# Optimization experiments

Hardware: AMD Instinct MI355X
Metric: run time of the kernel (lower is better)

The kernel has to match this reference:

```python
import jax, jax.numpy as jnp
import numpy as np

WS = 8
NH = 16
EPS = 1e-5

# relative position index (static, same as the torch buffer)
def _rel_index(ws):
    coords = np.stack(np.meshgrid(np.arange(ws), np.arange(ws), indexing='ij'))  # 2,ws,ws
    flat = coords.reshape(2, -1)
    rel = flat[:, :, None] - flat[:, None, :]
    rel = rel.transpose(1, 2, 0).copy()
    rel[..., 0] += ws - 1
    rel[..., 1] += ws - 1
    rel[..., 0] *= 2 * ws - 1
    return rel.sum(-1)  # (ws*ws, ws*ws)

REL_IDX = jnp.asarray(_rel_index(WS))

def conv2d(x, w, dilation=1, pad=None, groups=1):
    k = w.shape[-1]
    if pad is None:
        pad = (dilation * (k - 1)) // 2
    return jax.lax.conv_general_dilated(
        x, w, (1, 1), ((pad, pad), (pad, pad)), rhs_dilation=(dilation, dilation),
        dimension_numbers=('NCHW', 'OIHW', 'NCHW'), feature_group_count=groups)

def bn(x, p):
    g, b, m, v = p[0], p[1], p[2], p[3]
    inv = g / jnp.sqrt(v + EPS)
    return x * inv[:, None, None] + (b - m * inv)[:, None, None]

def avgpool(x, kh, kw, ph, pw):
    # torch AvgPool2d with count_include_pad=True: zero-pad then divide by kernel size
    s = jax.lax.reduce_window(x, 0.0, jax.lax.add, (1, 1, kh, kw), (1, 1, 1, 1),
                              ((0, 0), (0, 0), (ph, ph), (pw, pw)))
    return s / (kh * kw)

def _fwd(x, w_pre, bn_pre, w_l1, bn_l1, w_l2, bn_l2, w_l3, bn_l3, w_qkv, rpb, w_dw, w_pw, bn_proj):
    B, C, H, W = x.shape
    # local conv branch (chunk 256 -> 86,86,84 with dilations 1,2,3)
    local = bn(conv2d(x, w_pre), bn_pre)
    l1 = bn(conv2d(local[:, :86], w_l1, dilation=1), bn_l1)
    l2 = bn(conv2d(local[:, 86:172], w_l2, dilation=2), bn_l2)
    l3 = bn(conv2d(local[:, 172:], w_l3, dilation=3), bn_l3)
    local = jnp.concatenate([l1, l2, l3], axis=1)
    # pad to window multiple (reflect); static shapes so Python branch is fine
    ph, pw = (-H) % WS, (-W) % WS
    if ph or pw:
        x = jnp.pad(x, ((0, 0), (0, 0), (0, ph), (0, pw)), mode='reflect')
    Hp, Wp = H + ph, W + pw
    hh, ww = Hp // WS, Wp // WS
    d = C // NH
    qkv = conv2d(x, w_qkv)  # (B, 3C, Hp, Wp)
    qkv = qkv.reshape(B, 3, NH, d, hh, WS, ww, WS)
    qkv = qkv.transpose(1, 0, 4, 6, 2, 5, 7, 3).reshape(3, B * hh * ww, NH, WS * WS, d)
    q, k, v = qkv[0], qkv[1], qkv[2]
    dots = jnp.einsum('whid,whjd->whij', q, k) * (d ** -0.5)
    bias = rpb[REL_IDX.reshape(-1)].reshape(WS * WS, WS * WS, NH).transpose(2, 0, 1)
    attn = jax.nn.softmax(dots + bias[None], axis=-1)
    out = jnp.einsum('whij,whjd->whid', attn, v)
    out = out.reshape(B, hh, ww, NH, WS, WS, d).transpose(0, 3, 6, 1, 4, 2, 5).reshape(B, C, Hp, Wp)
    out = out[:, :, :H, :W]
    ax = avgpool(jnp.pad(out, ((0, 0), (0, 0), (0, 1), (0, 0)), mode='reflect'), WS, 1, WS // 2 - 1, 0)
    ay = avgpool(jnp.pad(out, ((0, 0), (0, 0), (0, 0), (0, 1)), mode='reflect'), 1, WS, 0, WS // 2 - 1)
    out = ax + ay + local
    out = jnp.pad(out, ((0, 0), (0, 0), (0, 1), (0, 1)), mode='reflect')
    out = conv2d(out, w_dw, pad=3, groups=C)       # depthwise 8x8
    out = bn(conv2d(out, w_pw), bn_proj)           # pointwise + BN
    return out[:, :, :H, :W]

def setup_inputs() -> dict:
    key = jax.random.key(0)
    ks = jax.random.split(key, 16)
    def w(k, shape, s=0.05):
        return jax.random.normal(k, shape, dtype=jnp.float32) * s
    def bnp(k, c):
        p = jax.random.uniform(k, (4, c), dtype=jnp.float32)
        return p.at[3].add(0.5)  # keep var positive and away from 0
    return {
        'x': jax.random.normal(ks[0], (8, 256, 128, 128), dtype=jnp.float32),
        'w_pre': w(ks[1], (256, 256, 1, 1)), 'bn_pre': bnp(ks[2], 256),
        'w_l1': w(ks[3], (86, 86, 3, 3)), 'bn_l1': bnp(ks[4], 86),
        'w_l2': w(ks[5], (86, 86, 3, 3)), 'bn_l2': bnp(ks[6], 86),
        'w_l3': w(ks[7], (84, 84, 3, 3)), 'bn_l3': bnp(ks[8], 84),
        'w_qkv': w(ks[9], (768, 256, 1, 1)),
        'rpb': w(ks[10], (225, 16), 0.02),
        'w_dw': w(ks[11], (256, 1, 8, 8)),
        'w_pw': w(ks[12], (256, 256, 1, 1)),
        'bn_proj': bnp(ks[13], 256),
    }

def reference(x, w_pre, bn_pre, w_l1, bn_l1, w_l2, bn_l2, w_l3, bn_l3, w_qkv, rpb, w_dw, w_pw, bn_proj):
    return _fwd(x, w_pre, bn_pre, w_l1, bn_l1, w_l2, bn_l2, w_l3, bn_l3, w_qkv, rpb, w_dw, w_pw, bn_proj)
```

## Files before the change

kernel.cpp:

```cpp
#include <hip/hip_runtime.h>
#include <hip/hip_bf16.h>
#include <cstdint>
#include <cstddef>

namespace {

constexpr int HW = 16384;

typedef short vec8s __attribute__((ext_vector_type(8)));
typedef float f32x4 __attribute__((ext_vector_type(4)));

__device__ __forceinline__ float u2f(uint32_t u){ union { uint32_t u; float f; } v; v.u = u; return v.f; }
__device__ __forceinline__ uint32_t f2u(float f){ union { float f; uint32_t u; } v; v.f = f; return v.u; }
__device__ __forceinline__ uint16_t f2bf(float f){
  uint32_t u = f2u(f);
  u += 0x7fffu + ((u >> 16) & 1u);
  return (uint16_t)(u >> 16);
}
__device__ __forceinline__ void unpack2(uint32_t w, float& lo, float& hi){
  lo = u2f(w << 16);
  hi = u2f(w & 0xffff0000u);
}

__global__ __launch_bounds__(256) void k_w2bf(
    const float* __restrict__ src, uint16_t* __restrict__ dst, int n)
{
  int i = (blockIdx.x * 256 + threadIdx.x) * 8;
  if (i + 8 <= n) {
    float4 a = *(const float4*)(src + i);
    float4 b = *(const float4*)(src + i + 4);
    uint4 pk;
    pk.x = (uint32_t)f2bf(a.x) | ((uint32_t)f2bf(a.y) << 16);
    pk.y = (uint32_t)f2bf(a.z) | ((uint32_t)f2bf(a.w) << 16);
    pk.z = (uint32_t)f2bf(b.x) | ((uint32_t)f2bf(b.y) << 16);
    pk.w = (uint32_t)f2bf(b.z) | ((uint32_t)f2bf(b.w) << 16);
    *(uint4*)(dst + i) = pk;
  }
}

template<int OUT_MODE, int NCO, bool WINM>
__global__ __launch_bounds__(256) void k_gemm_v4(
    const float* __restrict__ xf, const uint16_t* __restrict__ wbf,
    const float* __restrict__ bnp,
    uint16_t* __restrict__ outbPre, uint16_t* __restrict__ outbQkv,
    float* __restrict__ outf)
{
  __shared__ __align__(16) uint16_t sX[128][260];
  __shared__ __align__(16) uint16_t sW[128][36];
  const int t = threadIdx.x;
  const int b    = blockIdx.x >> 7;
  const int tile = blockIdx.x & 127;
  const int l = t & 63, w = t >> 6;
  const int l15 = l & 15, koct = l >> 4;
  const int wc = w >> 1, wp = w & 1;

  {
    const int cig = t >> 5;
    const int pq  = (t & 31) * 4;
    int gpx;
    if constexpr (WINM) {
      int win = tile * 2 + (pq >> 6);
      int p = pq & 63;
      gpx = ((win >> 4) * 8 + (p >> 3)) * 128 + (win & 15) * 8 + (p & 7);
    } else {
      gpx = tile * 128 + pq;
    }
    const float* srcb = xf + (size_t)b * 256 * HW + gpx;
    #pragma unroll
    for (int cb8 = 0; cb8 < 32; ++cb8) {
      int ci = cb8 * 8 + cig;
      float4 v = *(const float4*)(srcb + (size_t)ci * HW);
      sX[pq][ci]     = f2bf(v.x);
      sX[pq + 1][ci] = f2bf(v.y);
      sX[pq + 2][ci] = f2bf(v.z);
      sX[pq + 3][ci] = f2bf(v.w);
    }
  }

  const int swc = t >> 1, swh = t & 1;
  uint4 wr0, wr1;
  {
    const uint16_t* p = wbf + (size_t)swc * 256 + swh * 16;
    wr0 = *(const uint4*)(p);
    wr1 = *(const uint4*)(p + 8);
  }
  __syncthreads();

  for (int cc = 0; cc < NCO; ++cc) {
    f32x4 acc[4][4];
    #pragma unroll
    for (int cf = 0; cf < 4; ++cf)
      #pragma unroll
      for (int pf = 0; pf < 4; ++pf) acc[cf][pf] = (f32x4){0.f,0.f,0.f,0.f};

    for (int kc = 0; kc < 8; ++kc) {
      if (cc | kc) __syncthreads();
      {
        uint16_t* dst = &sW[swc][swh * 16];
        *(uint4*)(dst)     = wr0;
        *(uint4*)(dst + 8) = wr1;
      }
      {
        int nkc = kc + 1, ncc = cc;
        if (nkc == 8) { nkc = 0; ncc = cc + 1; }
        if (ncc < NCO) {
          const uint16_t* p = wbf + (size_t)(ncc * 128 + swc) * 256 + nkc * 32 + swh * 16;
          wr0 = *(const uint4*)(p);
          wr1 = *(const uint4*)(p + 8);
        }
      }
      __syncthreads();
      vec8s bf[4];
      #pragma unroll
      for (int pf = 0; pf < 4; ++pf)
        bf[pf] = *(const vec8s*)&sX[wp * 64 + pf * 16 + l15][kc * 32 + koct * 8];
      #pragma unroll
      for (int cf = 0; cf < 4; ++cf) {
        vec8s af = *(const vec8s*)&sW[wc * 64 + cf * 16 + l15][koct * 8];
        #pragma unroll
        for (int pf = 0; pf < 4; ++pf)
          acc[cf][pf] = __builtin_amdgcn_mfma_f32_16x16x32_bf16(af, bf[pf], acc[cf][pf], 0, 0, 0);
      }
    }

    #pragma unroll
    for (int cf = 0; cf < 4; ++cf) {
      const int cbase = cc * 128 + wc * 64 + cf * 16 + koct * 4;
      if constexpr (OUT_MODE == 2) {
        float scv[4], shv[4];
        #pragma unroll
        for (int r = 0; r < 4; ++r) {
          int c = cbase + r;
          float g = bnp[c], be = bnp[256 + c], mu = bnp[512 + c], va = bnp[768 + c];
          scv[r] = g * rsqrtf(va + 1e-5f);
          shv[r] = be - mu * scv[r];
        }
        #pragma unroll
        for (int pf = 0; pf < 4; ++pf) {
          int px = tile * 128 + wp * 64 + pf * 16 + l15;
          #pragma unroll
          for (int r = 0; r < 4; ++r)
            outf[(size_t)(b * 256 + cbase + r) * HW + px] =
                fmaf(acc[cf][pf][r], scv[r], shv[r]);
        }
      } else {
        if (cc < 2) {
          float scv[4], shv[4];
          #pragma unroll
          for (int r = 0; r < 4; ++r) {
            int c = cbase + r;
            float g = bnp[c], be = bnp[256 + c], mu = bnp[512 + c], va = bnp[768 + c];
            scv[r] = g * rsqrtf(va + 1e-5f);
            shv[r] = be - mu * scv[r];
          }
          #pragma unroll
          for (int pf = 0; pf < 4; ++pf) {
            int e = wp * 64 + pf * 16 + l15;
            int win = tile * 2 + (e >> 6);
            int p = e & 63;
            int gpx = ((win >> 4) * 8 + (p >> 3)) * 128 + (win & 15) * 8 + (p & 7);
            __align__(8) uint16_t pk[4];
            #pragma unroll
            for (int r = 0; r < 4; ++r)
              pk[r] = f2bf(fmaf(acc[cf][pf][r], scv[r], shv[r]));
            *(uint2*)(outbPre + ((size_t)b * HW + gpx) * 256 + cbase) = *(uint2*)pk;
          }
        } else {
          const int c0 = cbase - 256;
          #pragma unroll
          for (int pf = 0; pf < 4; ++pf) {
            int win = tile * 2 + wp;
            int p = pf * 16 + l15;
            uint16_t* dstp = outbQkv + ((size_t)(b * 256 + win) * 768 + c0) * 64 + p;
            #pragma unroll
            for (int r = 0; r < 4; ++r)
              dstp[(size_t)r * 64] = f2bf(acc[cf][pf][r]);
          }
        }
      }
    }
  }
}

template<int DIL, int CG>
__global__ __launch_bounds__(256) void k_dilconv_mfma(
    const uint16_t* __restrict__ preT, const float* __restrict__ wt,
    const float* __restrict__ bnp, float* __restrict__ out,
    int cb, int cb_al)
{
  constexpr int R = 8 + 2 * DIL;
  constexpr int C = 64 + 2 * DIL;
  constexpr int NPOS = R * C;
  constexpr int NIT = (NPOS + 255) / 256;
  __shared__ __align__(16) uint16_t sX[NPOS * 16];
  __shared__ __align__(16) uint16_t sW[10 * 50 * 16];

  const int t = threadIdx.x;
  const int rt    = blockIdx.x >> 1;
  const int ctile = blockIdx.x & 1;
  const int ct2   = blockIdx.y;
  const int b     = blockIdx.z;
  const int y0 = rt * 8, x0 = ctile * 64;
  const int l = t & 63, w = t >> 6;
  const int l15 = l & 15, oct = (l >> 4) & 1, half = l >> 5;
  const int rbase = w * 2;

  f32x4 acc[3][8];
  #pragma unroll
  for (int cf = 0; cf < 3; ++cf)
    #pragma unroll
    for (int q = 0; q < 8; ++q) acc[cf][q] = (f32x4){0.f,0.f,0.f,0.f};

  for (int kc = 0; kc < 6; ++kc) {
    #pragma unroll
    for (int i = 0; i < 3; ++i) {
      int pair = t + i * 256;
      int co = pair >> 4, ci = pair & 15;
      int cog = ct2 * 48 + co;
      int c = cb_al + kc * 16 + ci;
      bool ok = (cog < CG) && (c >= cb) && (c < cb + CG);
      size_t widx = ok ? ((size_t)cog * (size_t)CG + (size_t)(c - cb)) * 9u
                       : (size_t)0;
      const float* wp = wt + widx;
      uint16_t* dst = &sW[co * 16 + ci];
      #pragma unroll
      for (int tap = 0; tap < 9; ++tap)
        dst[tap * 800] = ok ? f2bf(wp[tap]) : (uint16_t)0;
      dst[9 * 800] = 0;
    }
    #pragma unroll
    for (int i = 0; i < NIT; ++i) {
      int p = t + i * 256;
      if (p < NPOS) {
        int row = p / C, col = p % C;
        int gy = y0 + row - DIL, gx = x0 + col - DIL;
        uint4 va = {0,0,0,0}, vb = {0,0,0,0};
        if ((unsigned)gy < 128u && (unsigned)gx < 128u) {
          const uint4* src = (const uint4*)(preT +
              (((size_t)b * HW + gy * 128 + gx) * 256 + cb_al + kc * 16));
          va = src[0]; vb = src[1];
        }
        uint4* dst = (uint4*)&sX[p * 16];
        dst[0] = va; dst[1] = vb;
      }
    }
    __syncthreads();

    #pragma unroll
    for (int s = 0; s < 5; ++s) {
      const int tap0 = 2 * s, tap1 = 2 * s + 1;
      const int dy0 = tap0 / 3, dx0 = tap0 % 3;
      const int dy1 = (tap1 <= 8) ? tap1 / 3 : 2;
      const int dx1 = (tap1 <= 8) ? tap1 % 3 : 2;
      const int dy = half ? dy1 : dy0;
      const int dx = half ? dx1 : dx0;
      const int atap = tap0 + half;
      vec8s a0 = *(const vec8s*)&sW[(atap * 50 + 0  + l15) * 16 + oct * 8];
      vec8s a1 = *(const vec8s*)&sW[(atap * 50 + 16 + l15) * 16 + oct * 8];
      vec8s a2 = *(const vec8s*)&sW[(atap * 50 + 32 + l15) * 16 + oct * 8];
      #pragma unroll
      for (int rs = 0; rs < 2; ++rs) {
        const int rowin = rbase + rs + dy * DIL;
        #pragma unroll
        for (int c4 = 0; c4 < 4; ++c4) {
          const int colin = c4 * 16 + l15 + dx * DIL;
          vec8s bf = *(const vec8s*)&sX[(rowin * C + colin) * 16 + oct * 8];
          acc[0][rs*4+c4] = __builtin_amdgcn_mfma_f32_16x16x32_bf16(a0, bf, acc[0][rs*4+c4], 0, 0, 0);
          acc[1][rs*4+c4] = __builtin_amdgcn_mfma_f32_16x16x32_bf16(a1, bf, acc[1][rs*4+c4], 0, 0, 0);
          acc[2][rs*4+c4] = __builtin_amdgcn_mfma_f32_16x16x32_bf16(a2, bf, acc[2][rs*4+c4], 0, 0, 0);
        }
      }
    }
    __syncthreads();
  }

  const int row4 = (l >> 4);
  #pragma unroll
  for (int cf = 0; cf < 3; ++cf) {
    #pragma unroll
    for (int r = 0; r < 4; ++r) {
      int c_loc = ct2 * 48 + cf * 16 + row4 * 4 + r;
      if (c_loc < CG) {
        int cg = cb + c_loc;
        float g = bnp[c_loc], be = bnp[CG + c_loc];
        float mu = bnp[2 * CG + c_loc], va = bnp[3 * CG + c_loc];
        float scv = g * rsqrtf(va + 1e-5f);
        float shv = be - mu * scv;
        #pragma unroll
        for (int rs = 0; rs < 2; ++rs) {
          int y = y0 + rbase + rs;
          #pragma unroll
          for (int c4 = 0; c4 < 4; ++c4) {
            int x = x0 + c4 * 16 + l15;
            out[(size_t)(b * 256 + cg) * HW + y * 128 + x] =
                fmaf(acc[cf][rs*4+c4][r], scv, shv);
          }
        }
      }
    }
  }
}

__global__ __launch_bounds__(256) void k_attn(
    const uint16_t* __restrict__ qkvW, const float* __restrict__ rpb,
    uint16_t* __restrict__ outp)
{
  __shared__ __align__(16) uint16_t sAll[4][5632];
  const int t = threadIdx.x;
  const int l = t & 63, w = t >> 6;
  const int l15 = l & 15, koct = l >> 4;
  const int b = blockIdx.y;
  const int win = blockIdx.x;
  const int wy = win >> 4, wx = win & 15;
  const int wbase = (wy * 8) * 128 + wx * 8;
  const uint16_t* base = qkvW + (size_t)(b * 256 + win) * 49152;
  uint16_t* swKT = &sAll[w][0];
  uint16_t* swQT = &sAll[w][2560];
  uint16_t* swPT = &sAll[w][0];
  float*    swO  = (float*)&sAll[w][0];
  float*    swB  = (float*)&sAll[w][5120];

  const uint16_t* qg = base + (size_t)(w * 16) * 64;
  const uint16_t* kg = qg + 256 * 64;
  const uint16_t* vg = qg + 512 * 64;
  uint32_t kp[8], qp[8];
  float breg[4];
  #pragma unroll
  for (int m = 0; m < 8; ++m) {
    uint32_t k0 = kg[(2 * m) * 64 + l], k1 = kg[(2 * m + 1) * 64 + l];
    uint32_t q0 = qg[(2 * m) * 64 + l], q1 = qg[(2 * m + 1) * 64 + l];
    kp[m] = k0 | (k1 << 16);
    qp[m] = q0 | (q1 << 16);
  }
  #pragma unroll
  for (int m = 0; m < 4; ++m) {
    int e = l + m * 64;
    breg[m] = (e < 225) ? rpb[e * 16 + w] : 0.f;
  }

  for (int it = 0; it < 4; ++it) {
    const int n = w + it * 4;
    #pragma unroll
    for (int m = 0; m < 4; ++m) {
      int e = l + m * 64;
      if (e < 225) swB[e] = breg[m];
    }
    {
      uint4 z = {0, 0, 0, 0};
      *(uint4*)(swKT + l * 40)      = *(uint4*)&kp[0];
      *(uint4*)(swKT + l * 40 + 8)  = *(uint4*)&kp[4];
      *(uint4*)(swKT + l * 40 + 16) = z;
      *(uint4*)(swKT + l * 40 + 24) = z;
      *(uint4*)(swQT + l * 40)      = *(uint4*)&qp[0];
      *(uint4*)(swQT + l * 40 + 8)  = *(uint4*)&qp[4];
      *(uint4*)(swQT + l * 40 + 16) = z;
      *(uint4*)(swQT + l * 40 + 24) = z;
    }
    vec8s vA0 = *(const vec8s*)(vg + l15 * 64 + koct * 8);
    vec8s vA1 = *(const vec8s*)(vg + l15 * 64 + 32 + koct * 8);
    if (it < 3) {
      const uint16_t* qg2 = qg + 4096;
      const uint16_t* kg2 = kg + 4096;
      #pragma unroll
      for (int m = 0; m < 8; ++m) {
        uint32_t k0 = kg2[(2 * m) * 64 + l], k1 = kg2[(2 * m + 1) * 64 + l];
        uint32_t q0 = qg2[(2 * m) * 64 + l], q1 = qg2[(2 * m + 1) * 64 + l];
        kp[m] = k0 | (k1 << 16);
        qp[m] = q0 | (q1 << 16);
      }
      #pragma unroll
      for (int m = 0; m < 4; ++m) {
        int e = l + m * 64;
        breg[m] = (e < 225) ? rpb[e * 16 + n + 4] : 0.f;
      }
    }
    asm volatile("s_waitcnt lgkmcnt(0)" ::: "memory");
    __builtin_amdgcn_sched_barrier(0);

    vec8s aK[4], bQ[4];
    #pragma unroll
    for (int tt = 0; tt < 4; ++tt) {
      aK[tt] = *(const vec8s*)(swKT + (tt * 16 + l15) * 40 + koct * 8);
      bQ[tt] = *(const vec8s*)(swQT + (tt * 16 + l15) * 40 + koct * 8);
    }
    f32x4 accS[4][4];
    #pragma unroll
    for (int ti = 0; ti < 4; ++ti)
      #pragma unroll
      for (int tj = 0; tj < 4; ++tj)
        accS[ti][tj] = __builtin_amdgcn_mfma_f32_16x16x32_bf16(
            aK[tj], bQ[ti], (f32x4){0.f, 0.f, 0.f, 0.f}, 0, 0, 0);

    float p[4][16], sinv[4];
    #pragma unroll
    for (int ti = 0; ti < 4; ++ti) {
      const int i = ti * 16 + l15;
      const int irow = i >> 3, icol = i & 7;
      #pragma unroll
      for (int tj = 0; tj < 4; ++tj) {
        #pragma unroll
        for (int r = 0; r < 4; ++r) {
          int j = tj * 16 + koct * 4 + r;
          int rel = (irow - (j >> 3) + 7) * 15 + (icol - (j & 7) + 7);
          p[ti][tj * 4 + r] = fmaf(accS[ti][tj][r], 0.25f, swB[rel]);
        }
      }
      float mx = p[ti][0];
      #pragma unroll
      for (int u = 1; u < 16; ++u) mx = fmaxf(mx, p[ti][u]);
      mx = fmaxf(mx, __shfl_xor(mx, 16));
      mx = fmaxf(mx, __shfl_xor(mx, 32));
      float s = 0.f;
      #pragma unroll
      for (int u = 0; u < 16; ++u) { p[ti][u] = __expf(p[ti][u] - mx); s += p[ti][u]; }
      s += __shfl_xor(s, 16);
      s += __shfl_xor(s, 32);
      sinv[ti] = 1.f / s;
    }

    #pragma unroll
    for (int ti = 0; ti < 4; ++ti) {
      uint16_t* rowp = swPT + (ti * 16 + l15) * 68 + koct * 4;
      #pragma unroll
      for (int tj = 0; tj < 4; ++tj) {
        uint32_t u0 = (uint32_t)f2bf(p[ti][tj * 4 + 0]) | ((uint32_t)f2bf(p[ti][tj * 4 + 1]) << 16);
        uint32_t u1 = (uint32_t)f2bf(p[ti][tj * 4 + 2]) | ((uint32_t)f2bf(p[ti][tj * 4 + 3]) << 16);
        *(uint32_t*)(rowp + tj * 16)     = u0;
        *(uint32_t*)(rowp + tj * 16 + 2) = u1;
      }
    }
    asm volatile("s_waitcnt lgkmcnt(0)" ::: "memory");
    __builtin_amdgcn_sched_barrier(0);

    f32x4 accO[4];
    #pragma unroll
    for (int ii = 0; ii < 4; ++ii) accO[ii] = (f32x4){0.f, 0.f, 0.f, 0.f};
    #pragma unroll
    for (int ks = 0; ks < 2; ++ks) {
      vec8s aV = ks ? vA1 : vA0;
      #pragma unroll
      for (int ii = 0; ii < 4; ++ii) {
        vec8s bP;
        const uint16_t* src = swPT + (ii * 16 + l15) * 68 + ks * 32 + koct * 8;
        *(uint2*)&bP       = *(const uint2*)(src);
        *((uint2*)&bP + 1) = *(const uint2*)(src + 4);
        accO[ii] = __builtin_amdgcn_mfma_f32_16x16x32_bf16(aV, bP, accO[ii], 0, 0, 0);
      }
    }
    asm volatile("s_waitcnt lgkmcnt(0)" ::: "memory");
    __builtin_amdgcn_sched_barrier(0);

    #pragma unroll
    for (int ii = 0; ii < 4; ++ii) {
      #pragma unroll
      for (int r = 0; r < 4; ++r) {
        int dd = koct * 4 + r;
        swO[dd * 76 + ii * 16 + l15] = accO[ii][r] * sinv[ii];
      }
    }
    asm volatile("s_waitcnt lgkmcnt(0)" ::: "memory");
    __builtin_amdgcn_sched_barrier(0);
    #pragma unroll
    for (int e2 = 0; e2 < 2; ++e2) {
      int e = l + e2 * 64;
      int dd = e >> 3, row = e & 7;
      const float* orow = swO + dd * 76 + row * 8;
      float4 a = *(const float4*)(orow);
      float4 c = *(const float4*)(orow + 4);
      uint4 pk;
      pk.x = (uint32_t)f2bf(a.x) | ((uint32_t)f2bf(a.y) << 16);
      pk.y = (uint32_t)f2bf(a.z) | ((uint32_t)f2bf(a.w) << 16);
      pk.z = (uint32_t)f2bf(c.x) | ((uint32_t)f2bf(c.y) << 16);
      pk.w = (uint32_t)f2bf(c.z) | ((uint32_t)f2bf(c.w) << 16);
      *(uint4*)(outp + (size_t)(b * 256 + n * 16 + dd) * HW + wbase + row * 128) = pk;
    }
    asm volatile("s_waitcnt lgkmcnt(0)" ::: "memory");
    __builtin_amdgcn_sched_barrier(0);
    qg += 4096; kg += 4096; vg += 4096;
  }
}

__global__ __launch_bounds__(256) void k_pool(
    const uint16_t* __restrict__ attnb, float* __restrict__ loc)
{
  __shared__ __align__(16) float sP[71][136];
  const int t = threadIdx.x;
  const int plane = blockIdx.x >> 1;
  const int h0 = (blockIdx.x & 1) * 64;
  const size_t pbase = (size_t)plane * HW;
  #pragma unroll
  for (int k = 0; k < 5; ++k) {
    int idx = t + k * 256;
    if (idx < 71 * 16) {
      int lr = idx >> 4, m = idx & 15;
      int g = h0 - 3 + lr;
      float f[8] = {0.f,0.f,0.f,0.f,0.f,0.f,0.f,0.f};
      if (g >= 0 && g <= 127) {
        uint4 v4 = *(const uint4*)(attnb + pbase + (size_t)g * 128 + m * 8);
        unpack2(v4.x, f[0], f[1]); unpack2(v4.y, f[2], f[3]);
        unpack2(v4.z, f[4], f[5]); unpack2(v4.w, f[6], f[7]);
      }
      float* dst = &sP[lr][4 + m * 8];
      *(float4*)dst       = (float4){f[0], f[1], f[2], f[3]};
      *(float4*)(dst + 4) = (float4){f[4], f[5], f[6], f[7]};
    }
  }
  #pragma unroll
  for (int k = 0; k < 3; ++k) {
    int idx = t + k * 256;
    if (idx < 71 * 8) {
      int lr = idx >> 3, e = idx & 7;
      int c = (e < 4) ? e : (128 + e);
      sP[lr][c] = 0.f;
    }
  }
  __syncthreads();

  const int q  = t & 31;
  const int r0 = (t >> 5) * 8;
  const int w0 = q * 4;
  float4 av = {0.f, 0.f, 0.f, 0.f};
  #pragma unroll
  for (int o = 0; o < 8; ++o) {
    float4 v = *(const float4*)&sP[r0 + o][4 + w0];
    av.x += v.x; av.y += v.y; av.z += v.z; av.w += v.w;
  }
  #pragma unroll
  for (int rr = 0; rr < 8; ++rr) {
    const int lh = r0 + rr;
    const int h = h0 + lh;
    float4 a = av;
    if (h >= 124) {
      float4 cfix = *(const float4*)&sP[126 - 64 + 3][4 + w0];
      a.x += cfix.x; a.y += cfix.y; a.z += cfix.z; a.w += cfix.w;
    }
    float4 hv0 = *(const float4*)&sP[lh + 3][w0];
    float4 hv1 = *(const float4*)&sP[lh + 3][w0 + 4];
    float4 hv2 = *(const float4*)&sP[lh + 3][w0 + 8];
    float s0 = hv0.y + hv0.z + hv0.w + hv1.x + hv1.y + hv1.z + hv1.w + hv2.x;
    float s1 = s0 - hv0.y + hv2.y;
    float s2 = s1 - hv0.z + hv2.z;
    float s3 = s2 - hv0.w + hv2.w;
    if (q == 31) {
      float cfix = sP[lh + 3][130];
      s0 += cfix; s1 += cfix; s2 += cfix; s3 += cfix;
    }
    const size_t gi = pbase + (size_t)h * 128 + w0;
    float4 lv = *(const float4*)(loc + gi);
    float4 o4;
    o4.x = fmaf(a.x + s0, 0.125f, lv.x);
    o4.y = fmaf(a.y + s1, 0.125f, lv.y);
    o4.z = fmaf(a.z + s2, 0.125f, lv.z);
    o4.w = fmaf(a.w + s3, 0.125f, lv.w);
    *(float4*)(loc + gi) = o4;
    if (rr < 7) {
      float4 vm = *(const float4*)&sP[lh][4 + w0];
      float4 vp = *(const float4*)&sP[lh + 8][4 + w0];
      av.x += vp.x - vm.x; av.y += vp.y - vm.y;
      av.z += vp.z - vm.z; av.w += vp.w - vm.w;
    }
  }
}

__global__ __launch_bounds__(256) void k_dw(
    const float* __restrict__ comb, const float* __restrict__ wdw,
    float* __restrict__ out)
{
  __shared__ __align__(16) float sZ[71][136];
  __shared__ float sWd[64];
  const int t = threadIdx.x;
  const int plane = blockIdx.x >> 1;
  const int cch = plane & 255;
  const int h0 = (blockIdx.x & 1) * 64;
  const size_t pbase = (size_t)plane * HW;
  if (t < 64) sWd[t] = wdw[cch * 64 + t];
  #pragma unroll
  for (int k = 0; k < 5; ++k) {
    int idx = t + k * 256;
    if (idx < 71 * 16) {
      int lr = idx >> 4, m = idx & 15;
      int g = h0 - 3 + lr;
      float4 a = {0.f,0.f,0.f,0.f}, c = {0.f,0.f,0.f,0.f};
      if (g >= 0 && g <= 128) {
        int gr = (g == 128) ? 126 : g;
        const float* src = comb + pbase + (size_t)gr * 128 + m * 8;
        a = *(const float4*)(src);
        c = *(const float4*)(src + 4);
      }
      float* dst = &sZ[lr][4 + m * 8];
      *(float4*)dst       = a;
      *(float4*)(dst + 4) = c;
    }
  }
  if (t < 71) {
    int lr = t;
    int g = h0 - 3 + lr;
    float rv = 0.f;
    if (g >= 0 && g <= 128) {
      int gr = (g == 128) ? 126 : g;
      rv = comb[pbase + (size_t)gr * 128 + 126];
    }
    *(float4*)&sZ[lr][0] = (float4){0.f, 0.f, 0.f, 0.f};
    sZ[lr][132] = rv;
    sZ[lr][133] = 0.f; sZ[lr][134] = 0.f; sZ[lr][135] = 0.f;
  }
  __syncthreads();

  float wt[8][8];
  #pragma unroll
  for (int i = 0; i < 8; ++i) {
    *(float4*)&wt[i][0] = *(const float4*)&sWd[i * 8];
    *(float4*)&wt[i][4] = *(const float4*)&sWd[i * 8 + 4];
  }

  const int q  = t & 31;
  const int rg = t >> 5;
  const int w0 = q * 4;
  f32x4 acc[8];
  #pragma unroll
  for (int rr = 0; rr < 8; ++rr) acc[rr] = (f32x4){0.f,0.f,0.f,0.f};

  #pragma unroll
  for (int v = 0; v < 15; ++v) {
    const int lr = rg * 8 + v;
    float win[12];
    *(float4*)&win[0] = *(const float4*)&sZ[lr][w0];
    *(float4*)&win[4] = *(const float4*)&sZ[lr][w0 + 4];
    *(float4*)&win[8] = *(const float4*)&sZ[lr][w0 + 8];
    #pragma unroll
    for (int rr = 0; rr < 8; ++rr) {
      const int i = v - rr;
      if (i >= 0 && i < 8) {
        #pragma unroll
        for (int c = 0; c < 4; ++c) {
          float s = acc[rr][c];
          #pragma unroll
          for (int j = 0; j < 8; ++j)
            s = fmaf(wt[i][j], win[c + j + 1], s);
          acc[rr][c] = s;
        }
      }
    }
  }
  #pragma unroll
  for (int rr = 0; rr < 8; ++rr) {
    int h = h0 + rg * 8 + rr;
    float* dst = out + pbase + (size_t)h * 128 + w0;
    *(float4*)dst = (float4){acc[rr][0], acc[rr][1], acc[rr][2], acc[rr][3]};
  }
}

}

extern "C" void kernel_launch(void* const* d_in, const int* in_sizes, int n_in,
                              void* d_out, int out_size, void* d_ws, size_t ws_size,
                              hipStream_t stream)
{
  const float* x      = (const float*)d_in[0];
  const float* w_pre  = (const float*)d_in[1];
  const float* bn_pre = (const float*)d_in[2];
  const float* w_l1   = (const float*)d_in[3];
  const float* bn_l1  = (const float*)d_in[4];
  const float* w_l2   = (const float*)d_in[5];
  const float* bn_l2  = (const float*)d_in[6];
  const float* w_l3   = (const float*)d_in[7];
  const float* bn_l3  = (const float*)d_in[8];
  const float* w_qkv  = (const float*)d_in[9];
  const float* rpb    = (const float*)d_in[10];
  const float* w_dw   = (const float*)d_in[11];
  const float* w_pw   = (const float*)d_in[12];
  const float* bn_pj  = (const float*)d_in[13];
  float* out = (float*)d_out;

  char* base = (char*)d_ws;
  uint16_t* preT  = (uint16_t*)(base + (size_t)67108864);
  float*    bufB  = (float*)(base + (size_t)134217728);
  uint16_t* bufQ  = (uint16_t*)(base + (size_t)268435456);
  uint16_t* attnO = preT;
  float*    bufDw = (float*)bufQ;
  uint16_t* wcomb_bf = (uint16_t*)out;
  uint16_t* wpw_bf   = preT;

  dim3 blk(256);
  k_w2bf<<<dim3(32),  blk, 0, stream>>>(w_pre, wcomb_bf, 65536);
  k_w2bf<<<dim3(96),  blk, 0, stream>>>(w_qkv, wcomb_bf + 65536, 196608);
  k_gemm_v4<4, 8, true><<<dim3(1024), blk, 0, stream>>>(
      x, wcomb_bf, bn_pre, preT, bufQ, nullptr);
  k_dilconv_mfma<1, 86><<<dim3(32, 2, 8), blk, 0, stream>>>(preT, w_l1, bn_l1, bufB, 0, 0);
  k_dilconv_mfma<2, 86><<<dim3(32, 2, 8), blk, 0, stream>>>(preT, w_l2, bn_l2, bufB, 86, 80);
  k_dilconv_mfma<3, 84><<<dim3(32, 2, 8), blk, 0, stream>>>(preT, w_l3, bn_l3, bufB, 172, 160);
  k_attn<<<dim3(256, 8), blk, 0, stream>>>(bufQ, rpb, attnO);
  k_pool<<<dim3(4096), blk, 0, stream>>>(attnO, bufB);
  k_w2bf<<<dim3(32), blk, 0, stream>>>(w_pw, wpw_bf, 65536);
  k_dw<<<dim3(4096), blk, 0, stream>>>(bufB, w_dw, bufDw);
  k_gemm_v4<2, 2, false><<<dim3(1024), blk, 0, stream>>>(
      bufDw, wpw_bf, bn_pj, nullptr, nullptr, out);

  (void)in_sizes; (void)n_in; (void)out_size; (void)ws_size;
}
```

Before: 642.7 us.

## Halve GEMM pixel tile to 64 and vectorize bf16 activation staging

The 1x1-conv GEMM kernel now processes 64 pixels (one window) per block instead of 128, doubling the grid to 2048 blocks. Each wave computes 32 output channels by 64 pixels instead of 64x64, which halves the accumulator registers. The activation load now has each thread gather 16 channels for 4 pixels and write them to LDS with 16-byte stores, replacing scattered 2-byte stores. This aims for higher occupancy and cheaper LDS staging, at the cost of reloading the weights twice as often per pixel and doing fewer MFMAs per weight fragment.

```diff
diff --git a/kernel.cpp b/kernel.cpp
--- a/kernel.cpp
+++ b/kernel.cpp
@@ -39,41 +39,45 @@
 }
 
 template<int OUT_MODE, int NCO, bool WINM>
-__global__ __launch_bounds__(256) void k_gemm_v4(
+__global__ __launch_bounds__(256) void k_gemm_v5(
     const float* __restrict__ xf, const uint16_t* __restrict__ wbf,
     const float* __restrict__ bnp,
     uint16_t* __restrict__ outbPre, uint16_t* __restrict__ outbQkv,
     float* __restrict__ outf)
 {
-  __shared__ __align__(16) uint16_t sX[128][260];
+  __shared__ __align__(16) uint16_t sX[64][266];
   __shared__ __align__(16) uint16_t sW[128][36];
   const int t = threadIdx.x;
-  const int b    = blockIdx.x >> 7;
-  const int tile = blockIdx.x & 127;
+  const int b    = blockIdx.x >> 8;
+  const int tile = blockIdx.x & 255;
   const int l = t & 63, w = t >> 6;
   const int l15 = l & 15, koct = l >> 4;
-  const int wc = w >> 1, wp = w & 1;
 
   {
-    const int cig = t >> 5;
-    const int pq  = (t & 31) * 4;
+    const int pqg = t & 15;
+    const int cig = t >> 4;
     int gpx;
     if constexpr (WINM) {
-      int win = tile * 2 + (pq >> 6);
-      int p = pq & 63;
-      gpx = ((win >> 4) * 8 + (p >> 3)) * 128 + (win & 15) * 8 + (p & 7);
+      int p = pqg * 4;
+      gpx = ((tile >> 4) * 8 + (p >> 3)) * 128 + (tile & 15) * 8 + (p & 7);
     } else {
-      gpx = tile * 128 + pq;
+      gpx = tile * 64 + pqg * 4;
     }
     const float* srcb = xf + (size_t)b * 256 * HW + gpx;
-    #pragma unroll
-    for (int cb8 = 0; cb8 < 32; ++cb8) {
-      int ci = cb8 * 8 + cig;
-      float4 v = *(const float4*)(srcb + (size_t)ci * HW);
-      sX[pq][ci]     = f2bf(v.x);
-      sX[pq + 1][ci] = f2bf(v.y);
-      sX[pq + 2][ci] = f2bf(v.z);
-      sX[pq + 3][ci] = f2bf(v.w);
+    __align__(16) uint16_t buf[4][16];
+    #pragma unroll
+    for (int co16 = 0; co16 < 16; ++co16) {
+      float4 v = *(const float4*)(srcb + (size_t)(cig * 16 + co16) * HW);
+      buf[0][co16] = f2bf(v.x);
+      buf[1][co16] = f2bf(v.y);
+      buf[2][co16] = f2bf(v.z);
+      buf[3][co16] = f2bf(v.w);
+    }
+    #pragma unroll
+    for (int pxl = 0; pxl < 4; ++pxl) {
+      uint16_t* dst = &sX[pqg * 4 + pxl][cig * 16];
+      *(uint4*)(dst)     = *(uint4*)&buf[pxl][0];
+      *(uint4*)(dst + 8) = *(uint4*)&buf[pxl][8];
     }
   }
 
@@ -87,9 +91,9 @@
   __syncthreads();
 
   for (int cc = 0; cc < NCO; ++cc) {
-    f32x4 acc[4][4];
-    #pragma unroll
-    for (int cf = 0; cf < 4; ++cf)
+    f32x4 acc[2][4];
+    #pragma unroll
+    for (int cf = 0; cf < 2; ++cf)
       #pragma unroll
       for (int pf = 0; pf < 4; ++pf) acc[cf][pf] = (f32x4){0.f,0.f,0.f,0.f};
 
@@ -113,10 +117,10 @@
       vec8s bf[4];
       #pragma unroll
       for (int pf = 0; pf < 4; ++pf)
-        bf[pf] = *(const vec8s*)&sX[wp * 64 + pf * 16 + l15][kc * 32 + koct * 8];
-      #pragma unroll
-      for (int cf = 0; cf < 4; ++cf) {
-        vec8s af = *(const vec8s*)&sW[wc * 64 + cf * 16 + l15][koct * 8];
+        bf[pf] = *(const vec8s*)&sX[pf * 16 + l15][kc * 32 + koct * 8];
+      #pragma unroll
+      for (int cf = 0; cf < 2; ++cf) {
+        vec8s af = *(const vec8s*)&sW[w * 32 + cf * 16 + l15][koct * 8];
         #pragma unroll
         for (int pf = 0; pf < 4; ++pf)
           acc[cf][pf] = __builtin_amdgcn_mfma_f32_16x16x32_bf16(af, bf[pf], acc[cf][pf], 0, 0, 0);
@@ -124,8 +128,8 @@
     }
 
     #pragma unroll
-    for (int cf = 0; cf < 4; ++cf) {
-      const int cbase = cc * 128 + wc * 64 + cf * 16 + koct * 4;
+    for (int cf = 0; cf < 2; ++cf) {
+      const int cbase = cc * 128 + w * 32 + cf * 16 + koct * 4;
       if constexpr (OUT_MODE == 2) {
         float scv[4], shv[4];
         #pragma unroll
@@ -137,7 +141,7 @@
         }
         #pragma unroll
         for (int pf = 0; pf < 4; ++pf) {
-          int px = tile * 128 + wp * 64 + pf * 16 + l15;
+          int px = tile * 64 + pf * 16 + l15;
           #pragma unroll
           for (int r = 0; r < 4; ++r)
             outf[(size_t)(b * 256 + cbase + r) * HW + px] =
@@ -155,10 +159,8 @@
           }
           #pragma unroll
           for (int pf = 0; pf < 4; ++pf) {
-            int e = wp * 64 + pf * 16 + l15;
-            int win = tile * 2 + (e >> 6);
-            int p = e & 63;
-            int gpx = ((win >> 4) * 8 + (p >> 3)) * 128 + (win & 15) * 8 + (p & 7);
+            int e = pf * 16 + l15;
+            int gpx = ((tile >> 4) * 8 + (e >> 3)) * 128 + (tile & 15) * 8 + (e & 7);
             __align__(8) uint16_t pk[4];
             #pragma unroll
             for (int r = 0; r < 4; ++r)
@@ -169,9 +171,8 @@
           const int c0 = cbase - 256;
           #pragma unroll
           for (int pf = 0; pf < 4; ++pf) {
-            int win = tile * 2 + wp;
             int p = pf * 16 + l15;
-            uint16_t* dstp = outbQkv + ((size_t)(b * 256 + win) * 768 + c0) * 64 + p;
+            uint16_t* dstp = outbQkv + ((size_t)(b * 256 + tile) * 768 + c0) * 64 + p;
             #pragma unroll
             for (int r = 0; r < 4; ++r)
               dstp[(size_t)r * 64] = f2bf(acc[cf][pf][r]);
@@ -684,7 +685,7 @@
   dim3 blk(256);
   k_w2bf<<<dim3(32),  blk, 0, stream>>>(w_pre, wcomb_bf, 65536);
   k_w2bf<<<dim3(96),  blk, 0, stream>>>(w_qkv, wcomb_bf + 65536, 196608);
-  k_gemm_v4<4, 8, true><<<dim3(1024), blk, 0, stream>>>(
+  k_gemm_v5<4, 8, true><<<dim3(2048), blk, 0, stream>>>(
       x, wcomb_bf, bn_pre, preT, bufQ, nullptr);
   k_dilconv_mfma<1, 86><<<dim3(32, 2, 8), blk, 0, stream>>>(preT, w_l1, bn_l1, bufB, 0, 0);
   k_dilconv_mfma<2, 86><<<dim3(32, 2, 8), blk, 0, stream>>>(preT, w_l2, bn_l2, bufB, 86, 80);
@@ -693,7 +694,7 @@
   k_pool<<<dim3(4096), blk, 0, stream>>>(attnO, bufB);
   k_w2bf<<<dim3(32), blk, 0, stream>>>(w_pw, wpw_bf, 65536);
   k_dw<<<dim3(4096), blk, 0, stream>>>(bufB, w_dw, bufDw);
-  k_gemm_v4<2, 2, false><<<dim3(1024), blk, 0, stream>>>(
+  k_gemm_v5<2, 2, false><<<dim3(2048), blk, 0, stream>>>(
       bufDw, wpw_bf, bn_pj, nullptr, nullptr, out);
 
   (void)in_sizes; (void)n_in; (void)out_size; (void)ws_size;
```

Result: slower. 758.6 us (+18.0%).
